# Kernel optimization log

Hardware: AMD Instinct MI355X
Metric: run time of the kernel (lower is better)

Reference implementation:

```python
import jax, jax.numpy as jnp
import numpy as np

B, N1, N2, E = 8, 32, 32, 256
H = 8                 # num_heads == args.vir_heads
KD = E // H           # key dim per head = 32
HD = E // H           # head dim (value_dim == embed_dim)
L = N1 * N2           # 1024 tokens
SCALING = KD ** -0.5
LN_EPS = 1e-5


def _rel_pos_2d():
    # RetNetRelPosDeform2D with zero offsets (vir_use_deformable=False)
    half = 1.0 / 10000.0 ** jnp.linspace(0.0, 1.0, KD // 2)
    angle = jnp.repeat(half, 2)                                   # (KD,) interleaved pairs
    decay = jnp.log(1.0 - 2.0 ** (-2.0 - 5.0 * jnp.arange(H, dtype=jnp.float32) / H))  # (H,)
    i1 = jnp.arange(N1, dtype=jnp.float32)
    i2 = jnp.arange(N2, dtype=jnp.float32)
    index_k = (i1[:, None] + i2[None, :]).reshape(L)              # (L,)
    sin_k = jnp.sin(index_k[:, None] * angle[None, :])            # (L, KD)
    cos_k = jnp.cos(index_k[:, None] * angle[None, :])
    # zero offsets => index_q == index_k, broadcast over (B, H)
    sin_q = sin_k[None, None]                                     # (1,1,L,KD)
    cos_q = cos_k[None, None]
    # Manhattan distance decay mask on the 2D grid
    d = (jnp.abs(i1[:, None, None, None] - i1[None, None, :, None])
         + jnp.abs(i2[None, :, None, None] - i2[None, None, None, :])).reshape(L, L)
    mask = jnp.exp(d[None, :, :] * decay[:, None, None])          # (H, L, L)
    mask = jnp.nan_to_num(mask)
    mask = mask / jnp.sqrt(mask.sum(-1, keepdims=True))
    return sin_q, cos_q, sin_k, cos_k, mask


def rotate_every_two(x):
    x1 = x[..., ::2]
    x2 = x[..., 1::2]
    return jnp.stack((-x2, x1), axis=-1).reshape(x.shape)


def theta_shift(x, sin, cos):
    return x * cos + rotate_every_two(x) * sin


def setup_inputs() -> dict:
    key = jax.random.key(0)
    ks = jax.random.split(key, 5)
    gain_qkv = 2.0 ** -2.5 * (6.0 / (E + E)) ** 0.5  # xavier_uniform bound scale
    gain_o = 2.0 ** -1 * (6.0 / (E + E)) ** 0.5
    x = jax.random.normal(ks[0], (B, N1, N2, E), dtype=jnp.float32)
    Wq = jax.random.uniform(ks[1], (E, E), jnp.float32, -gain_qkv, gain_qkv)
    Wk = jax.random.uniform(ks[2], (E, E), jnp.float32, -gain_qkv, gain_qkv)
    Wv = jax.random.uniform(ks[3], (E, E), jnp.float32, -gain_qkv, gain_qkv)
    Wo = jax.random.uniform(ks[4], (E, E), jnp.float32, -gain_o, gain_o)
    ln_g = jnp.ones((HD,), jnp.float32)
    ln_b = jnp.zeros((HD,), jnp.float32)
    return {"x": x, "Wq": Wq, "Wk": Wk, "Wv": Wv, "Wo": Wo, "ln_g": ln_g, "ln_b": ln_b}


def reference(x, Wq, Wk, Wv, Wo, ln_g, ln_b):
    sin_q, cos_q, sin_k, cos_k, mask = _rel_pos_2d()
    xf = x.reshape(B, L, E)
    q = (xf @ Wq.T).reshape(B, L, H, KD).transpose(0, 2, 1, 3)    # (B,H,L,KD)
    k = (xf @ Wk.T * SCALING).reshape(B, L, H, KD).transpose(0, 2, 1, 3)
    vr = (xf @ Wv.T).reshape(B, L, H, HD).transpose(0, 2, 1, 3)   # (B,H,L,HD)
    qr = theta_shift(q, sin_q, cos_q)
    kr = theta_shift(k, sin_k[None, None], cos_k[None, None])
    qk = jnp.einsum('bhqd,bhkd->bhqk', qr, kr) * mask[None]       # (B,H,L,L)
    den = jnp.clip(jax.lax.stop_gradient(jnp.abs(qk)).sum(-1, keepdims=True), 1.0, 5e4)
    qk = qk / den
    out = jnp.einsum('bhqk,bhkd->bhqd', qk, vr).transpose(0, 2, 1, 3)  # (B,L,H,HD)
    mu = out.mean(-1, keepdims=True)
    var = out.var(-1, keepdims=True)
    out = (out - mu) / jnp.sqrt(var + LN_EPS) * ln_g + ln_b       # per-head LayerNorm
    out = jax.nn.gelu(out.reshape(B, L, H * HD), approximate=False)
    out = out @ Wo.T
    return out.reshape(B, N1, N2, E)
```

## Files before the change

### kernel.cpp

```cpp
#include <hip/hip_runtime.h>
#include <math.h>

typedef unsigned short u16;
typedef unsigned int u32;
typedef unsigned long long u64;
typedef __bf16 bf16x8 __attribute__((ext_vector_type(8)));
typedef short s16x4 __attribute__((ext_vector_type(4)));
typedef float f32x4 __attribute__((ext_vector_type(4)));

#define SCALING 0.17677669529663687f
#define LOG2E 1.44269504088896f
#define LOG2_10000 13.287712379549449f

__device__ __forceinline__ u16 f2bf(float f) {
    u32 u; __builtin_memcpy(&u, &f, 4);
    u = u + 0x7FFFu + ((u >> 16) & 1u);
    return (u16)(u >> 16);
}
__device__ __forceinline__ u32 fbits(float f) {
    u32 u; __builtin_memcpy(&u, &f, 4); return u;
}
__device__ __forceinline__ u32 pack_bf16(float lo, float hi) {
#if __has_builtin(__builtin_amdgcn_cvt_pk_bf16_f32)
    typedef __bf16 bf16x2_t __attribute__((ext_vector_type(2)));
    bf16x2_t r = __builtin_amdgcn_cvt_pk_bf16_f32(lo, hi);
    u32 u; __builtin_memcpy(&u, &r, 4); return u;
#else
    return __builtin_amdgcn_perm(fbits(hi) + 0x8000u, fbits(lo) + 0x8000u, 0x07060302u);
#endif
}
__device__ __forceinline__ f32x4 mfma16(bf16x8 a, bf16x8 b, f32x4 c) {
    return __builtin_amdgcn_mfma_f32_16x16x32_bf16(a, b, c, 0, 0, 0);
}
__device__ __forceinline__ f32x4 mfma_k16(u64 a, u64 b, f32x4 c) {
#if __has_builtin(__builtin_amdgcn_mfma_f32_16x16x16bf16_1k)
    s16x4 av, bv;
    __builtin_memcpy(&av, &a, 8); __builtin_memcpy(&bv, &b, 8);
    return __builtin_amdgcn_mfma_f32_16x16x16bf16_1k(av, bv, c, 0, 0, 0);
#elif __has_builtin(__builtin_amdgcn_mfma_f32_16x16x16_bf16)
    typedef __bf16 bf16x4_t __attribute__((ext_vector_type(4)));
    bf16x4_t av, bv;
    __builtin_memcpy(&av, &a, 8); __builtin_memcpy(&bv, &b, 8);
    return __builtin_amdgcn_mfma_f32_16x16x16_bf16(av, bv, c, 0, 0, 0);
#else
    f32x4 d = c;
    asm volatile("v_mfma_f32_16x16x16_bf16 %0, %1, %2, %0\n\ts_nop 4"
                 : "+v"(d) : "v"(a), "v"(b));
    return d;
#endif
}
__device__ __forceinline__ float decay_l2(int h) {
    return logf(1.0f - exp2f(-2.0f - 0.625f * (float)h)) * LOG2E;
}

__global__ __launch_bounds__(256) void prep_kernel(
    const float* __restrict__ x,
    const float* __restrict__ Wq, const float* __restrict__ Wk,
    const float* __restrict__ Wv, const float* __restrict__ Wo,
    u16* __restrict__ xb, u16* __restrict__ wb, float2* __restrict__ tc) {
    int bid = blockIdx.x;
    if (bid >= 1152) {
        int idx = (bid - 1152) * 256 + threadIdx.x;
        int l = idx >> 5, d = idx & 31;
        float ang = exp2f(-LOG2_10000 * (1.0f / 15.0f) * (float)(d >> 1));
        float idl = (float)((l >> 5) + (l & 31));
        float sv, cv;
        __sincosf(idl * ang, &sv, &cv);
        tc[idx] = make_float2(cv, (d & 1) ? sv : -sv);
        return;
    }
    const float* src; u16* dst; int off;
    if (bid < 1024) { src = x; dst = xb; off = bid * 2048; }
    else {
        int wsel = (bid - 1024) >> 5;
        src = (wsel == 0) ? Wq : (wsel == 1) ? Wk : (wsel == 2) ? Wv : Wo;
        dst = wb + wsel * 65536;
        off = ((bid - 1024) & 31) * 2048;
    }
    int i = off + threadIdx.x * 8;
    float4 a = *(const float4*)&src[i];
    float4 b = *(const float4*)&src[i + 4];
    int4 t;
    t.x = (int)pack_bf16(a.x, a.y); t.y = (int)pack_bf16(a.z, a.w);
    t.z = (int)pack_bf16(b.x, b.y); t.w = (int)pack_bf16(b.z, b.w);
    *(int4*)&dst[i] = t;
}

template<int MT>
__global__ __launch_bounds__(256) void gemm_bt_kernel(
    const u16* __restrict__ A, const u16* __restrict__ Wb,
    const float2* __restrict__ tc,
    u16* __restrict__ O0, u16* __restrict__ O1, u16* __restrict__ O2,
    float* __restrict__ Of, int mode_base) {
    __shared__ __align__(16) u16 As[64 * MT * 136];
    __shared__ __align__(16) u16 Ws[64 * 136];
    int z = blockIdx.z;
    const u16* W = Wb + z * 65536;
    u16* O = (z == 0) ? O0 : (z == 1) ? O1 : O2;
    int mode = mode_base + z;
    int n0 = blockIdx.x * 64, r0 = blockIdx.y * (64 * MT);
    int tid = threadIdx.x;
    int w = tid >> 6, lane = tid & 63, ln = lane & 15, quad = lane >> 4;
    f32x4 acc[MT][4] = {};
#pragma unroll
    for (int ch = 0; ch < 2; ch++) {
        int k0 = ch * 128;
        if (ch) __syncthreads();
#pragma unroll
        for (int i = 0; i < 4 * MT; i++) {
            int c = tid + i * 256;
            int row = c >> 4, seg = c & 15;
            *(int4*)&As[row * 136 + seg * 8] = *(const int4*)&A[(long)(r0 + row) * 256 + k0 + seg * 8];
        }
#pragma unroll
        for (int i = 0; i < 4; i++) {
            int c = tid + i * 256;
            int row = c >> 4, seg = c & 15;
            *(int4*)&Ws[row * 136 + seg * 8] = *(const int4*)&W[(long)(n0 + row) * 256 + k0 + seg * 8];
        }
        __syncthreads();
#pragma unroll
        for (int kt = 0; kt < 4; kt++) {
            bf16x8 a[MT];
#pragma unroll
            for (int m = 0; m < MT; m++)
                a[m] = *(const bf16x8*)&As[(w * MT * 16 + m * 16 + ln) * 136 + kt * 32 + quad * 8];
#pragma unroll
            for (int nt = 0; nt < 4; nt++) {
                bf16x8 b = *(const bf16x8*)&Ws[(nt * 16 + ln) * 136 + kt * 32 + quad * 8];
#pragma unroll
                for (int m = 0; m < MT; m++)
                    acc[m][nt] = mfma16(a[m], b, acc[m][nt]);
            }
        }
    }
#pragma unroll
    for (int m = 0; m < MT; m++) {
        int rowg = r0 + w * MT * 16 + m * 16 + quad * 4;
        if (mode == 3) {
#pragma unroll
            for (int nt = 0; nt < 4; nt++) {
                int e = n0 + nt * 16 + ln;
#pragma unroll
                for (int r = 0; r < 4; r++)
                    Of[(long)(rowg + r) * 256 + e] = acc[m][nt][r];
            }
            continue;
        }
        float scl = (mode == 1) ? SCALING : 1.0f;
#pragma unroll
        for (int nt = 0; nt < 4; nt++) {
            int e = n0 + nt * 16 + ln;
            int d = e & 31, hh = e >> 5;
#pragma unroll
            for (int r = 0; r < 4; r++) {
                int gi = rowg + r;
                int b = gi >> 10, l = gi & 1023;
                float v = acc[m][nt][r] * scl;
                float p = __shfl_xor(v, 1);
                float res;
                if (mode == 2) {
                    res = v;
                } else {
                    float2 sc = tc[l * 32 + d];
                    res = v * sc.x + p * sc.y;
                }
                O[(((long)(b * 8 + hh)) * 1024 + l) * 32 + d] = f2bf(res);
            }
        }
    }
}

__global__ __launch_bounds__(512) void attn_kernel(
    const u16* __restrict__ qr, const u16* __restrict__ kr, const u16* __restrict__ vr,
    const float* __restrict__ lng, const float* __restrict__ lnb,
    u16* __restrict__ out) {
    __shared__ __align__(16) u16 Qs[128 * 40];
    __shared__ __align__(16) u16 Ks[2][64 * 40];
    __shared__ __align__(16) u32 VtW[2][32 * 36];
    __shared__ float Tt[64];
    __shared__ float Ss[32];
    int b = blockIdx.z, h = blockIdx.y, q0 = blockIdx.x * 128;
    int tid = threadIdx.x, w = tid >> 6, lane = tid & 63, ln = lane & 15, quad = lane >> 4;
    long bh = b * 8 + h;
    const u16* qb = qr + bh * 32768;
    const u16* kb = kr + bh * 32768;
    const u16* vb = vr + bh * 32768;
    float dec = decay_l2(h);
    {
        int row = tid >> 2, seg = tid & 3;
        *(int4*)&Qs[row * 40 + seg * 8] = *(const int4*)&qb[(q0 + row) * 32 + seg * 8];
    }
    if (tid < 63) Tt[tid] = exp2f(dec * (float)tid);
    bool isK = (tid < 256);
    int krow = (tid & 255) >> 2, kseg = tid & 3;
    int vt = tid & 255, vp = vt >> 3, vseg = vt & 7;
    int4 kreg; int2 v0, v1;
    if (isK) {
        kreg = *(const int4*)&kb[(long)krow * 32 + kseg * 8];
    } else {
        v0 = *(const int2*)&vb[(long)(vp * 2) * 32 + vseg * 4];
        v1 = *(const int2*)&vb[(long)(vp * 2 + 1) * 32 + vseg * 4];
    }
    __syncthreads();
    bf16x8 aq = *(const bf16x8*)&Qs[(w * 16 + ln) * 40 + quad * 8];
    int q = q0 + w * 16 + ln;
    int q1i = q >> 5, q2i = q & 31;
    if (tid < 32) {
        float s = 0.0f;
#pragma unroll
        for (int b2 = 0; b2 < 32; b2++) s += Tt[abs(tid - b2)];
        Ss[tid] = s;
    }
    if (isK) {
        *(int4*)&Ks[0][krow * 40 + kseg * 8] = kreg;
    } else {
        VtW[0][(vseg * 4 + 0) * 36 + vp] = __builtin_amdgcn_perm(v1.x, v0.x, 0x05040100u);
        VtW[0][(vseg * 4 + 1) * 36 + vp] = __builtin_amdgcn_perm(v1.x, v0.x, 0x07060302u);
        VtW[0][(vseg * 4 + 2) * 36 + vp] = __builtin_amdgcn_perm(v1.y, v0.y, 0x05040100u);
        VtW[0][(vseg * 4 + 3) * 36 + vp] = __builtin_amdgcn_perm(v1.y, v0.y, 0x07060302u);
    }
    __syncthreads();
    float rqv = rsqrtf(Ss[q1i] * Ss[q2i]);
    float bt[2][4];
#pragma unroll
    for (int s2 = 0; s2 < 2; s2++)
#pragma unroll
        for (int r = 0; r < 4; r++)
            bt[s2][r] = Tt[abs(q2i - (s2 * 16 + quad * 4 + r))] * rqv;
    f32x4 accO0 = {}, accO1 = {};
    float den = 0.0f;
    for (int kt = 0; kt < 16; kt++) {
        int cur = kt & 1;
        if (kt < 15) {
            long t1 = (long)(kt + 1) * 64;
            if (isK) {
                kreg = *(const int4*)&kb[(t1 + krow) * 32 + kseg * 8];
            } else {
                v0 = *(const int2*)&vb[(t1 + vp * 2) * 32 + vseg * 4];
                v1 = *(const int2*)&vb[(t1 + vp * 2 + 1) * 32 + vseg * 4];
            }
        }
        float a0 = Tt[abs(q1i - 2 * kt)];
        float a1 = Tt[abs(q1i - 2 * kt - 1)];
        const u16* ksb = &Ks[cur][0];
        const u32* vtb = &VtW[cur][0];
#pragma unroll
        for (int nt = 0; nt < 4; nt++) {
            bf16x8 ak = *(const bf16x8*)&ksb[(nt * 16 + ln) * 40 + quad * 8];
            f32x4 s = mfma16(ak, aq, (f32x4){0.f, 0.f, 0.f, 0.f});
            float aa = (nt & 2) ? a1 : a0;
            float p0 = s[0] * aa * bt[nt & 1][0];
            float p1 = s[1] * aa * bt[nt & 1][1];
            float p2 = s[2] * aa * bt[nt & 1][2];
            float p3 = s[3] * aa * bt[nt & 1][3];
            den += fabsf(p0); den += fabsf(p1); den += fabsf(p2); den += fabsf(p3);
            u32 blo = pack_bf16(p0, p1), bhi = pack_bf16(p2, p3);
            u64 bb = ((u64)bhi << 32) | blo;
            u64 av0 = *(const u64*)&vtb[ln * 36 + nt * 8 + quad * 2];
            u64 av1 = *(const u64*)&vtb[(16 + ln) * 36 + nt * 8 + quad * 2];
            accO0 = mfma_k16(av0, bb, accO0);
            accO1 = mfma_k16(av1, bb, accO1);
        }
        if (kt < 15) {
            int nb = 1 - cur;
            if (isK) {
                *(int4*)&Ks[nb][krow * 40 + kseg * 8] = kreg;
            } else {
                VtW[nb][(vseg * 4 + 0) * 36 + vp] = __builtin_amdgcn_perm(v1.x, v0.x, 0x05040100u);
                VtW[nb][(vseg * 4 + 1) * 36 + vp] = __builtin_amdgcn_perm(v1.x, v0.x, 0x07060302u);
                VtW[nb][(vseg * 4 + 2) * 36 + vp] = __builtin_amdgcn_perm(v1.y, v0.y, 0x05040100u);
                VtW[nb][(vseg * 4 + 3) * 36 + vp] = __builtin_amdgcn_perm(v1.y, v0.y, 0x07060302u);
            }
            __syncthreads();
        }
    }
    den += __shfl_xor(den, 16);
    den += __shfl_xor(den, 32);
    float id = 1.0f / fminf(fmaxf(den, 1.0f), 50000.0f);
    float o[8];
#pragma unroll
    for (int r = 0; r < 4; r++) { o[r] = accO0[r] * id; o[4 + r] = accO1[r] * id; }
    float s1 = 0.0f, s2 = 0.0f;
#pragma unroll
    for (int i = 0; i < 8; i++) { s1 += o[i]; s2 += o[i] * o[i]; }
    s1 += __shfl_xor(s1, 16); s1 += __shfl_xor(s1, 32);
    s2 += __shfl_xor(s2, 16); s2 += __shfl_xor(s2, 32);
    float mean = s1 * (1.0f / 32.0f);
    float var = s2 * (1.0f / 32.0f) - mean * mean;
    float rstd = rsqrtf(var + 1e-5f);
    float xg[8];
#pragma unroll
    for (int nv = 0; nv < 2; nv++)
#pragma unroll
        for (int r = 0; r < 4; r++) {
            int d = nv * 16 + quad * 4 + r;
            float xv = (o[nv * 4 + r] - mean) * rstd * lng[d] + lnb[d];
            xg[nv * 4 + r] = 0.5f * xv * (1.0f + erff(xv * 0.70710678118654752f));
        }
    u16* orow = out + ((long)(b * 1024 + q)) * 256 + h * 32;
    int2 st0, st1;
    st0.x = (int)pack_bf16(xg[0], xg[1]); st0.y = (int)pack_bf16(xg[2], xg[3]);
    st1.x = (int)pack_bf16(xg[4], xg[5]); st1.y = (int)pack_bf16(xg[6], xg[7]);
    *(int2*)&orow[quad * 4] = st0;
    *(int2*)&orow[16 + quad * 4] = st1;
}

extern "C" void kernel_launch(void* const* d_in, const int* in_sizes, int n_in,
                              void* d_out, int out_size, void* d_ws, size_t ws_size,
                              hipStream_t stream) {
    const float* x   = (const float*)d_in[0];
    const float* Wq  = (const float*)d_in[1];
    const float* Wk  = (const float*)d_in[2];
    const float* Wv  = (const float*)d_in[3];
    const float* Wo  = (const float*)d_in[4];
    const float* lng = (const float*)d_in[5];
    const float* lnb = (const float*)d_in[6];
    float* outp = (float*)d_out;

    u16* xb    = (u16*)d_ws;
    u16* wb    = xb + 2097152;
    u16* qr    = wb + 262144;
    u16* kr    = qr + 2097152;
    u16* vr    = kr + 2097152;
    u16* attnb = vr + 2097152;
    float2* tc = (float2*)(attnb + 2097152);

    prep_kernel<<<1280, 256, 0, stream>>>(x, Wq, Wk, Wv, Wo, xb, wb, tc);
    gemm_bt_kernel<1><<<dim3(4, 128, 3), 256, 0, stream>>>(xb, wb, tc, qr, kr, vr, nullptr, 0);
    attn_kernel<<<dim3(8, 8, 8), 512, 0, stream>>>(qr, kr, vr, lng, lnb, attnb);
    gemm_bt_kernel<1><<<dim3(4, 128, 1), 256, 0, stream>>>(attnb, wb + 3 * 65536, tc, nullptr, nullptr, nullptr, outp, 3);
}
```

Baseline: 112.7 us.

## Process two query tiles per warp in attention and remap blocks across XCDs

Each attention block now covers 256 queries instead of 128. Every warp handles two 16-row query tiles, so each K/V tile staged in shared memory is reused twice and block count halves. Blocks are remapped so consecutive (b,h) pairs sharing K/V land on the same XCD for L2 locality, and the QKV projection GEMM switches to its template variant 2 with half the grid in y. This costs more registers per thread and cuts parallelism to 256 attention blocks.

Result: slower. 116.8 us (+3.6%).

```diff
diff --git a/kernel.cpp b/kernel.cpp
--- a/kernel.cpp
+++ b/kernel.cpp
@@ -175,20 +175,25 @@
     const u16* __restrict__ qr, const u16* __restrict__ kr, const u16* __restrict__ vr,
     const float* __restrict__ lng, const float* __restrict__ lnb,
     u16* __restrict__ out) {
-    __shared__ __align__(16) u16 Qs[128 * 40];
+    __shared__ __align__(16) u16 Qs[256 * 40];
     __shared__ __align__(16) u16 Ks[2][64 * 40];
     __shared__ __align__(16) u32 VtW[2][32 * 36];
     __shared__ float Tt[64];
     __shared__ float Ss[32];
-    int b = blockIdx.z, h = blockIdx.y, q0 = blockIdx.x * 128;
+    int p = blockIdx.x + 4 * (blockIdx.y + 8 * blockIdx.z);
+    int xcd = p & 7, slot = p >> 3;
+    int c = xcd * 8 + (slot >> 2);
+    int b = c >> 3, h = c & 7, q0 = (slot & 3) * 256;
     int tid = threadIdx.x, w = tid >> 6, lane = tid & 63, ln = lane & 15, quad = lane >> 4;
     long bh = b * 8 + h;
     const u16* qb = qr + bh * 32768;
     const u16* kb = kr + bh * 32768;
     const u16* vb = vr + bh * 32768;
     float dec = decay_l2(h);
-    {
-        int row = tid >> 2, seg = tid & 3;
+#pragma unroll
+    for (int i = 0; i < 2; i++) {
+        int cc = tid + i * 512;
+        int row = cc >> 2, seg = cc & 3;
         *(int4*)&Qs[row * 40 + seg * 8] = *(const int4*)&qb[(q0 + row) * 32 + seg * 8];
     }
     if (tid < 63) Tt[tid] = exp2f(dec * (float)tid);
@@ -203,9 +208,11 @@
         v1 = *(const int2*)&vb[(long)(vp * 2 + 1) * 32 + vseg * 4];
     }
     __syncthreads();
-    bf16x8 aq = *(const bf16x8*)&Qs[(w * 16 + ln) * 40 + quad * 8];
-    int q = q0 + w * 16 + ln;
-    int q1i = q >> 5, q2i = q & 31;
+    bf16x8 aq0 = *(const bf16x8*)&Qs[(w * 32 + ln) * 40 + quad * 8];
+    bf16x8 aq1 = *(const bf16x8*)&Qs[(w * 32 + 16 + ln) * 40 + quad * 8];
+    int qA = q0 + w * 32 + ln;
+    int q1i = qA >> 5;
+    int q2i0 = qA & 31, q2i1 = (qA + 16) & 31;
     if (tid < 32) {
         float s = 0.0f;
 #pragma unroll
@@ -221,15 +228,19 @@
         VtW[0][(vseg * 4 + 3) * 36 + vp] = __builtin_amdgcn_perm(v1.y, v0.y, 0x07060302u);
     }
     __syncthreads();
-    float rqv = rsqrtf(Ss[q1i] * Ss[q2i]);
-    float bt[2][4];
+    float rqv0 = rsqrtf(Ss[q1i] * Ss[q2i0]);
+    float rqv1 = rsqrtf(Ss[q1i] * Ss[q2i1]);
+    float bt[2][2][4];
 #pragma unroll
     for (int s2 = 0; s2 < 2; s2++)
 #pragma unroll
-        for (int r = 0; r < 4; r++)
-            bt[s2][r] = Tt[abs(q2i - (s2 * 16 + quad * 4 + r))] * rqv;
-    f32x4 accO0 = {}, accO1 = {};
-    float den = 0.0f;
+        for (int r = 0; r < 4; r++) {
+            int kk = s2 * 16 + quad * 4 + r;
+            bt[0][s2][r] = Tt[abs(q2i0 - kk)] * rqv0;
+            bt[1][s2][r] = Tt[abs(q2i1 - kk)] * rqv1;
+        }
+    f32x4 accO[2][2] = {};
+    float den[2] = {0.0f, 0.0f};
     for (int kt = 0; kt < 16; kt++) {
         int cur = kt & 1;
         if (kt < 15) {
@@ -248,19 +259,25 @@
 #pragma unroll
         for (int nt = 0; nt < 4; nt++) {
             bf16x8 ak = *(const bf16x8*)&ksb[(nt * 16 + ln) * 40 + quad * 8];
-            f32x4 s = mfma16(ak, aq, (f32x4){0.f, 0.f, 0.f, 0.f});
+            f32x4 s0 = mfma16(ak, aq0, (f32x4){0.f, 0.f, 0.f, 0.f});
+            f32x4 s1 = mfma16(ak, aq1, (f32x4){0.f, 0.f, 0.f, 0.f});
             float aa = (nt & 2) ? a1 : a0;
-            float p0 = s[0] * aa * bt[nt & 1][0];
-            float p1 = s[1] * aa * bt[nt & 1][1];
-            float p2 = s[2] * aa * bt[nt & 1][2];
-            float p3 = s[3] * aa * bt[nt & 1][3];
-            den += fabsf(p0); den += fabsf(p1); den += fabsf(p2); den += fabsf(p3);
-            u32 blo = pack_bf16(p0, p1), bhi = pack_bf16(p2, p3);
-            u64 bb = ((u64)bhi << 32) | blo;
             u64 av0 = *(const u64*)&vtb[ln * 36 + nt * 8 + quad * 2];
             u64 av1 = *(const u64*)&vtb[(16 + ln) * 36 + nt * 8 + quad * 2];
-            accO0 = mfma_k16(av0, bb, accO0);
-            accO1 = mfma_k16(av1, bb, accO1);
+#pragma unroll
+            for (int u = 0; u < 2; u++) {
+                f32x4 s = u ? s1 : s0;
+                float p0 = s[0] * aa * bt[u][nt & 1][0];
+                float p1 = s[1] * aa * bt[u][nt & 1][1];
+                float p2 = s[2] * aa * bt[u][nt & 1][2];
+                float p3 = s[3] * aa * bt[u][nt & 1][3];
+                den[u] += fabsf(p0); den[u] += fabsf(p1);
+                den[u] += fabsf(p2); den[u] += fabsf(p3);
+                u32 blo = pack_bf16(p0, p1), bhi = pack_bf16(p2, p3);
+                u64 bb = ((u64)bhi << 32) | blo;
+                accO[u][0] = mfma_k16(av0, bb, accO[u][0]);
+                accO[u][1] = mfma_k16(av1, bb, accO[u][1]);
+            }
         }
         if (kt < 15) {
             int nb = 1 - cur;
@@ -275,35 +292,40 @@
             __syncthreads();
         }
     }
-    den += __shfl_xor(den, 16);
-    den += __shfl_xor(den, 32);
-    float id = 1.0f / fminf(fmaxf(den, 1.0f), 50000.0f);
-    float o[8];
-#pragma unroll
-    for (int r = 0; r < 4; r++) { o[r] = accO0[r] * id; o[4 + r] = accO1[r] * id; }
-    float s1 = 0.0f, s2 = 0.0f;
-#pragma unroll
-    for (int i = 0; i < 8; i++) { s1 += o[i]; s2 += o[i] * o[i]; }
-    s1 += __shfl_xor(s1, 16); s1 += __shfl_xor(s1, 32);
-    s2 += __shfl_xor(s2, 16); s2 += __shfl_xor(s2, 32);
-    float mean = s1 * (1.0f / 32.0f);
-    float var = s2 * (1.0f / 32.0f) - mean * mean;
-    float rstd = rsqrtf(var + 1e-5f);
-    float xg[8];
-#pragma unroll
-    for (int nv = 0; nv < 2; nv++)
-#pragma unroll
-        for (int r = 0; r < 4; r++) {
-            int d = nv * 16 + quad * 4 + r;
-            float xv = (o[nv * 4 + r] - mean) * rstd * lng[d] + lnb[d];
-            xg[nv * 4 + r] = 0.5f * xv * (1.0f + erff(xv * 0.70710678118654752f));
-        }
-    u16* orow = out + ((long)(b * 1024 + q)) * 256 + h * 32;
-    int2 st0, st1;
-    st0.x = (int)pack_bf16(xg[0], xg[1]); st0.y = (int)pack_bf16(xg[2], xg[3]);
-    st1.x = (int)pack_bf16(xg[4], xg[5]); st1.y = (int)pack_bf16(xg[6], xg[7]);
-    *(int2*)&orow[quad * 4] = st0;
-    *(int2*)&orow[16 + quad * 4] = st1;
+#pragma unroll
+    for (int u = 0; u < 2; u++) {
+        float dn = den[u];
+        dn += __shfl_xor(dn, 16);
+        dn += __shfl_xor(dn, 32);
+        float id = 1.0f / fminf(fmaxf(dn, 1.0f), 50000.0f);
+        float o[8];
+#pragma unroll
+        for (int r = 0; r < 4; r++) { o[r] = accO[u][0][r] * id; o[4 + r] = accO[u][1][r] * id; }
+        float s1 = 0.0f, s2 = 0.0f;
+#pragma unroll
+        for (int i = 0; i < 8; i++) { s1 += o[i]; s2 += o[i] * o[i]; }
+        s1 += __shfl_xor(s1, 16); s1 += __shfl_xor(s1, 32);
+        s2 += __shfl_xor(s2, 16); s2 += __shfl_xor(s2, 32);
+        float mean = s1 * (1.0f / 32.0f);
+        float var = s2 * (1.0f / 32.0f) - mean * mean;
+        float rstd = rsqrtf(var + 1e-5f);
+        float xg[8];
+#pragma unroll
+        for (int nv = 0; nv < 2; nv++)
+#pragma unroll
+            for (int r = 0; r < 4; r++) {
+                int d = nv * 16 + quad * 4 + r;
+                float xv = (o[nv * 4 + r] - mean) * rstd * lng[d] + lnb[d];
+                xg[nv * 4 + r] = 0.5f * xv * (1.0f + erff(xv * 0.70710678118654752f));
+            }
+        int q = qA + u * 16;
+        u16* orow = out + ((long)(b * 1024 + q)) * 256 + h * 32;
+        int2 st0, st1;
+        st0.x = (int)pack_bf16(xg[0], xg[1]); st0.y = (int)pack_bf16(xg[2], xg[3]);
+        st1.x = (int)pack_bf16(xg[4], xg[5]); st1.y = (int)pack_bf16(xg[6], xg[7]);
+        *(int2*)&orow[quad * 4] = st0;
+        *(int2*)&orow[16 + quad * 4] = st1;
+    }
 }
 
 extern "C" void kernel_launch(void* const* d_in, const int* in_sizes, int n_in,
@@ -327,7 +349,7 @@
     float2* tc = (float2*)(attnb + 2097152);
 
     prep_kernel<<<1280, 256, 0, stream>>>(x, Wq, Wk, Wv, Wo, xb, wb, tc);
-    gemm_bt_kernel<1><<<dim3(4, 128, 3), 256, 0, stream>>>(xb, wb, tc, qr, kr, vr, nullptr, 0);
-    attn_kernel<<<dim3(8, 8, 8), 512, 0, stream>>>(qr, kr, vr, lng, lnb, attnb);
+    gemm_bt_kernel<2><<<dim3(4, 64, 3), 256, 0, stream>>>(xb, wb, tc, qr, kr, vr, nullptr, 0);
+    attn_kernel<<<dim3(4, 8, 8), 512, 0, stream>>>(qr, kr, vr, lng, lnb, attnb);
     gemm_bt_kernel<1><<<dim3(4, 128, 1), 256, 0, stream>>>(attnb, wb + 3 * 65536, tc, nullptr, nullptr, nullptr, outp, 3);
 }
```
